# Kernel optimization log

Measured on AMD Instinct MI355X. Metric: run time of the kernel, lower is better.

## Reference

```python
import jax, jax.numpy as jnp
import numpy as np

N = 100000      # nodes
E = 800000      # edges
P = 200000      # number of subgraph permutations
L = 16          # lrp_length
D = 64          # lrp_out_dim (== lrp_in_dim)
PL = P * L
LEN_SEQ = 4     # int(sqrt(L))
NUM_BOND = 4


def setup_inputs() -> dict:
    key = jax.random.key(0)
    ks = jax.random.split(key, 16)
    inp = {}
    inp["nfeat"] = jax.random.normal(ks[0], (N, D), jnp.float32)
    inp["degs"] = jax.random.uniform(ks[1], (N,), jnp.float32) * 8.0 + 1.0
    inp["n2p_val"] = jnp.ones((PL,), jnp.float32)
    inp["e2p_val"] = jnp.ones((PL,), jnp.float32)
    inp["pool_val"] = jax.random.uniform(ks[2], (P,), jnp.float32)
    inp["weights"] = jax.random.normal(ks[3], (D, D, L), jnp.float32)
    inp["bias"] = jnp.zeros((1, D), jnp.float32)
    inp["w_deg0"] = jax.random.normal(ks[4], (2 * D, LEN_SEQ), jnp.float32) * 0.3
    inp["b_deg0"] = jnp.zeros((2 * D,), jnp.float32)
    inp["w_deg1"] = jax.random.normal(ks[5], (D, 2 * D), jnp.float32) * 0.1
    inp["b_deg1"] = jnp.zeros((D,), jnp.float32)
    inp["w_lin"] = jax.random.normal(ks[6], (D, D), jnp.float32) * 0.1
    inp["b_lin"] = jnp.zeros((D,), jnp.float32)
    inp["bond_emb"] = jax.random.normal(ks[7], (NUM_BOND, D), jnp.float32)
    inp["edge_feat_idx"] = jax.random.randint(ks[8], (E,), 0, NUM_BOND, jnp.int32)
    inp["n2p_row"] = jnp.arange(PL, dtype=jnp.int32)
    inp["n2p_col"] = jax.random.randint(ks[9], (PL,), 0, N, jnp.int32)
    inp["e2p_row"] = jnp.arange(PL, dtype=jnp.int32)
    inp["e2p_col"] = jax.random.randint(ks[10], (PL,), 0, E, jnp.int32)
    inp["pool_row"] = jax.random.randint(ks[11], (P,), 0, N, jnp.int32)
    inp["pool_col"] = jnp.arange(P, dtype=jnp.int32)
    return inp


def _spmm(row, col, val, x, m):
    # COO spmm: out[r] = sum_{nnz with row==r} val * x[col]
    return jax.ops.segment_sum(val[:, None] * x[col], row, num_segments=m)


def reference(nfeat, degs, n2p_val, e2p_val, pool_val, weights, bias,
              w_deg0, b_deg0, w_deg1, b_deg1, w_lin, b_lin, bond_emb,
              edge_feat_idx, n2p_row, n2p_col, e2p_row, e2p_col,
              pool_row, pool_col):
    n = nfeat.shape[0]
    pl = n2p_row.shape[0]
    d = weights.shape[0]
    l = weights.shape[2]
    p = pl // l
    len_seq = int(round(l ** 0.5))

    efeat = bond_emb[edge_feat_idx]                                  # [E, D]
    perm = _spmm(n2p_row, n2p_col, n2p_val, nfeat, pl) \
         + _spmm(e2p_row, e2p_col, e2p_val, efeat, pl)               # [P*L, D]
    deg_perm = _spmm(n2p_row, n2p_col, n2p_val, degs[:, None], pl)   # [P*L, 1]

    x = perm.reshape(p, l, d)                                        # [P, L, D]
    deg_sel = deg_perm.reshape(p, l)[:, ::len_seq + 1]               # [P, len_seq]

    h = jnp.einsum('pab,bca->pc', x, weights) + bias                 # [P, D]
    h = jax.nn.relu(h) @ w_lin.T + b_lin                             # linear(relu(.))

    g = jax.nn.relu(deg_sel @ w_deg0.T + b_deg0) @ w_deg1.T + b_deg1  # [P, D]
    h = h * g

    out = _spmm(pool_row, pool_col, pool_val, h, n)                  # [N, D]
    return out
```

## Files before the change

kernel.cpp:

```cpp
#include <hip/hip_runtime.h>
#include <hip/hip_bf16.h>

typedef __attribute__((ext_vector_type(8))) __bf16 bf16x8;
typedef __attribute__((ext_vector_type(4))) float floatx4;
typedef __attribute__((ext_vector_type(4))) int intx4;

constexpr int N_NODES = 100000;
constexpr int P_PERM  = 200000;

constexpr size_t W2F_OFF  = 0;
constexpr size_t WLF_OFF  = 131072;
constexpr size_t WD1F_OFF = 139264;
constexpr size_t BE_OFF   = 155648;
constexpr size_t NFBF_OFF = 3355648;
constexpr size_t H2_OFF   = 16155648;
constexpr size_t RP_OFF   = 67355648;
constexpr size_t CUR_OFF  = 67755664;
constexpr size_t CIDX_OFF = 68155664;
constexpr size_t CSUM_OFF = 68955664;
constexpr size_t WS_NEED_BF16 = 16155648;
constexpr size_t WS_NEED_CSR  = 68956000;

constexpr int SCAN_CHUNK = 2048;
constexpr int NCHUNK = 49;

__global__ void prep_all_kernel(float4* __restrict__ out,
                                const float* __restrict__ weights,
                                const float* __restrict__ w_lin,
                                const float* __restrict__ w_deg1,
                                const float* __restrict__ nfeat,
                                const int* __restrict__ e2p_col,
                                const int* __restrict__ edge_feat_idx,
                                __bf16* __restrict__ ws_bf,
                                int do_zero_out) {
  int b = blockIdx.x;
  int t = threadIdx.x;
  if (b < 6250) {
    if (do_zero_out) out[b * 256 + t] = make_float4(0.f, 0.f, 0.f, 0.f);
  } else if (b < 6554) {
    int i = (b - 6250) * 256 + t;
    if (i < 65536) {
      int j = i & 7, l = (i >> 3) & 63, ct = (i >> 9) & 3, ks = (i >> 11) & 1, a = i >> 12;
      int k = ks * 32 + (l >> 4) * 8 + j;
      int c = ct * 16 + (l & 15);
      ws_bf[W2F_OFF / 2 + i] = (__bf16)weights[k * 1024 + c * 16 + a];
    } else if (i < 65536 + 4096) {
      int i2 = i - 65536;
      int j = i2 & 7, l = (i2 >> 3) & 63, ct = (i2 >> 9) & 3, ks = (i2 >> 11) & 1;
      int k = ks * 32 + (l >> 4) * 8 + j;
      int c = ct * 16 + (l & 15);
      ws_bf[WLF_OFF / 2 + i2] = (__bf16)w_lin[c * 64 + k];
    } else if (i < 65536 + 4096 + 8192) {
      int i3 = i - 65536 - 4096;
      int j = i3 & 7, l = (i3 >> 3) & 63, ct = (i3 >> 9) & 3, ks = (i3 >> 11) & 3;
      int k = ks * 32 + (l >> 4) * 8 + j;
      int c = ct * 16 + (l & 15);
      ws_bf[WD1F_OFF / 2 + i3] = (__bf16)w_deg1[c * 128 + k];
    }
  } else if (b < 9679) {
    int i = (b - 6554) * 256 + t;
    if (i < N_NODES * 8) {
      float4 a = *(const float4*)(nfeat + (size_t)i * 8);
      float4 c = *(const float4*)(nfeat + (size_t)i * 8 + 4);
      bf16x8 o;
      o[0] = (__bf16)a.x; o[1] = (__bf16)a.y; o[2] = (__bf16)a.z; o[3] = (__bf16)a.w;
      o[4] = (__bf16)c.x; o[5] = (__bf16)c.y; o[6] = (__bf16)c.z; o[7] = (__bf16)c.w;
      *(bf16x8*)(ws_bf + NFBF_OFF / 2 + (size_t)i * 8) = o;
    }
  } else if (b < 12804) {
    int i = (b - 9679) * 256 + t;
    if (i < P_PERM * 4) {
      int4 ec = ((const int4*)e2p_col)[i];
      unsigned v = (unsigned)(edge_feat_idx[ec.x] & 0xff)
                 | ((unsigned)(edge_feat_idx[ec.y] & 0xff) << 8)
                 | ((unsigned)(edge_feat_idx[ec.z] & 0xff) << 16)
                 | ((unsigned)(edge_feat_idx[ec.w] & 0xff) << 24);
      ((unsigned*)((char*)ws_bf + BE_OFF))[i] = v;
    }
  } else {
    int i = (b - 12804) * 256 + t;
    if (i < N_NODES) ((int*)((char*)ws_bf + CUR_OFF))[i] = 0;
  }
}

__global__ void hist_kernel(const int* __restrict__ pool_row, int* __restrict__ hist) {
  int i = blockIdx.x * 256 + threadIdx.x;
  if (i < P_PERM) atomicAdd(&hist[pool_row[i]], 1);
}

__global__ void scan1_kernel(const int* __restrict__ hist, int* __restrict__ csum) {
  __shared__ int red[256];
  int b = blockIdx.x, t = threadIdx.x;
  int s = 0;
  #pragma unroll
  for (int j = 0; j < 8; ++j) {
    int i = b * SCAN_CHUNK + t * 8 + j;
    s += (i < N_NODES) ? hist[i] : 0;
  }
  red[t] = s;
  __syncthreads();
  for (int off = 128; off > 0; off >>= 1) {
    if (t < off) red[t] += red[t + off];
    __syncthreads();
  }
  if (t == 0) csum[b] = red[0];
}

__global__ void scan2_kernel(int* __restrict__ csum, int* __restrict__ row_ptr) {
  if (threadIdx.x == 0) {
    int acc = 0;
    for (int i = 0; i < NCHUNK; ++i) {
      int v = csum[i];
      csum[i] = acc;
      acc += v;
    }
    row_ptr[N_NODES] = acc;
  }
}

__global__ void scan3_kernel(const int* __restrict__ csum,
                             int* __restrict__ hist_cursor,
                             int* __restrict__ row_ptr) {
  __shared__ int sc[257];
  int b = blockIdx.x, t = threadIdx.x;
  int v[8];
  int s = 0;
  #pragma unroll
  for (int j = 0; j < 8; ++j) {
    int i = b * SCAN_CHUNK + t * 8 + j;
    v[j] = (i < N_NODES) ? hist_cursor[i] : 0;
    s += v[j];
  }
  sc[t + 1] = s;
  if (t == 0) sc[0] = 0;
  __syncthreads();
  for (int off = 1; off < 256; off <<= 1) {
    int x = (t >= off) ? sc[t + 1 - off] : 0;
    __syncthreads();
    sc[t + 1] += x;
    __syncthreads();
  }
  int excl = csum[b] + sc[t];
  #pragma unroll
  for (int j = 0; j < 8; ++j) {
    int i = b * SCAN_CHUNK + t * 8 + j;
    if (i < N_NODES) {
      row_ptr[i] = excl;
      hist_cursor[i] = excl;
    }
    excl += v[j];
  }
}

__global__ void scatter_kernel(const int* __restrict__ pool_row,
                               int* __restrict__ cursor,
                               int* __restrict__ cidx) {
  int i = blockIdx.x * 256 + threadIdx.x;
  if (i < P_PERM) {
    int pos = atomicAdd(&cursor[pool_row[i]], 1);
    cidx[pos] = i;
  }
}

__global__ __launch_bounds__(256, 8) void pool_kernel(
    const int* __restrict__ row_ptr, const int* __restrict__ cidx,
    const float* __restrict__ pool_val, const float* __restrict__ h2,
    float* __restrict__ out) {
  int g = blockIdx.x * 256 + threadIdx.x;
  int n = g >> 2, qd = g & 3;
  if (n >= N_NODES) return;
  int s = row_ptr[n], e = row_ptr[n + 1];
  floatx4 a0 = {0,0,0,0}, a1 = {0,0,0,0}, a2 = {0,0,0,0}, a3 = {0,0,0,0};
  for (int i = s; i < e; ++i) {
    int p = cidx[i];
    float pv = pool_val[p];
    const float* hr = h2 + (size_t)p * 64 + qd * 16;
    floatx4 h0 = *(const floatx4*)(hr + 0);
    floatx4 h1 = *(const floatx4*)(hr + 4);
    floatx4 h2v = *(const floatx4*)(hr + 8);
    floatx4 h3 = *(const floatx4*)(hr + 12);
    a0 += pv * h0; a1 += pv * h1; a2 += pv * h2v; a3 += pv * h3;
  }
  float* orow = out + (size_t)n * 64 + qd * 16;
  *(floatx4*)(orow + 0) = a0;
  *(floatx4*)(orow + 4) = a1;
  *(floatx4*)(orow + 8) = a2;
  *(floatx4*)(orow + 12) = a3;
}

template <bool BF16FEAT, bool CSR>
__global__ __launch_bounds__(256, 4) void lrp_mfma_kernel(
    const float* __restrict__ nfeat,
    const float* __restrict__ degs,
    const float* __restrict__ n2p_val,
    const float* __restrict__ e2p_val,
    const float* __restrict__ pool_val,
    const float* __restrict__ bias,
    const float* __restrict__ w_deg0,
    const float* __restrict__ b_deg0,
    const float* __restrict__ b_deg1,
    const float* __restrict__ b_lin,
    const float* __restrict__ bond_emb,
    const int* __restrict__ n2p_col,
    const int* __restrict__ pool_row,
    const __bf16* __restrict__ ws_bf,
    float* __restrict__ h2out,
    float* __restrict__ out) {
  __shared__ __align__(16) char fraglds[2][8192];
  __shared__ __align__(16) __bf16 sbond[4][72];
  __shared__ __align__(16) float swdeg0[128][4];
  __shared__ float sbd0[128];
  __shared__ float sbias[64];
  __shared__ float sblin[64];
  __shared__ float sbd1[64];
  __shared__ __align__(16) __bf16 hs[4][2][16][72];

  const int t = threadIdx.x;
  const int w = t >> 6;
  const int l = t & 63;
  const int m = l & 15;
  const int q = l >> 4;
  const int pbase = blockIdx.x * 128 + w * 32;
  int pb[2] = {pbase, pbase + 16};
  bool valid[2];
  int pbc[2];
  #pragma unroll
  for (int pt = 0; pt < 2; ++pt) {
    valid[pt] = pb[pt] < P_PERM;
    pbc[pt] = valid[pt] ? pb[pt] : (P_PERM - 16);
  }

  if (t < 256) sbond[t >> 6][t & 63] = (__bf16)bond_emb[t];
  if (t < 128) {
    *(float4*)&swdeg0[t][0] = *(const float4*)(w_deg0 + t * 4);
    sbd0[t] = b_deg0[t];
  } else if (t < 192) {
    int c = t - 128;
    sbias[c] = bias[c]; sblin[c] = b_lin[c]; sbd1[c] = b_deg1[c];
  }

  const __bf16* __restrict__ nfbf = ws_bf + NFBF_OFF / 2;
  const bf16x8* __restrict__ WLv  = (const bf16x8*)(ws_bf + WLF_OFF / 2);
  const bf16x8* __restrict__ WD1v = (const bf16x8*)(ws_bf + WD1F_OFF / 2);
  const unsigned* __restrict__ bep = (const unsigned*)((const char*)ws_bf + BE_OFF);
  const char* __restrict__ W2bytes = (const char*)ws_bf + W2F_OFF;

  intx4 nvx[2], evx[2], ncx[2];
  int bex[2];
  #pragma unroll
  for (int pt = 0; pt < 2; ++pt) {
    size_t rb = (size_t)pbc[pt] * 16;
    nvx[pt] = *(const intx4*)(n2p_val + rb + 4 * l);
    evx[pt] = *(const intx4*)(e2p_val + rb + 4 * l);
    ncx[pt] = *(const intx4*)(n2p_col + rb + 4 * l);
    bex[pt] = (int)bep[(size_t)pbc[pt] * 4 + l];
  }
  const int selbase = m * 16;

  auto stage = [&](int a, int buf) {
    #pragma unroll
    for (int j = 0; j < 2; ++j) {
      const char* g = W2bytes + (size_t)a * 8192 + (w * 2 + j) * 1024 + l * 16;
      char* lds = &fraglds[buf][(w * 2 + j) * 1024];
      __builtin_amdgcn_global_load_lds(
          (const __attribute__((address_space(1))) unsigned*)g,
          (__attribute__((address_space(3))) unsigned*)lds, 16, 0, 0);
    }
  };
  auto gath = [&](int nc, bf16x8* g) {
    #pragma unroll
    for (int ks = 0; ks < 2; ++ks) {
      int k0 = ks * 32 + q * 8;
      if (BF16FEAT) {
        g[ks] = *(const bf16x8*)(nfbf + (size_t)nc * 64 + k0);
      } else {
        float4 n0 = *(const float4*)(nfeat + (size_t)nc * 64 + k0);
        float4 n1 = *(const float4*)(nfeat + (size_t)nc * 64 + k0 + 4);
        bf16x8 o;
        o[0] = (__bf16)n0.x; o[1] = (__bf16)n0.y; o[2] = (__bf16)n0.z; o[3] = (__bf16)n0.w;
        o[4] = (__bf16)n1.x; o[5] = (__bf16)n1.y; o[6] = (__bf16)n1.z; o[7] = (__bf16)n1.w;
        g[ks] = o;
      }
    }
  };

  floatx4 acc[2][4] = {};
  float dsreg[2][4];
  float nv0[2], ev0[2];
  int nc0[2], be0[2];
  bf16x8 g_cur[2][2], g_nxt[2][2];

  #pragma unroll
  for (int pt = 0; pt < 2; ++pt) {
    nv0[pt] = __int_as_float(__builtin_amdgcn_ds_bpermute(selbase, nvx[pt][0]));
    ev0[pt] = __int_as_float(__builtin_amdgcn_ds_bpermute(selbase, evx[pt][0]));
    nc0[pt] = __builtin_amdgcn_ds_bpermute(selbase, ncx[pt][0]);
    be0[pt] = (__builtin_amdgcn_ds_bpermute(selbase, bex[pt])) & 0xff;
    gath(nc0[pt], g_cur[pt]);
  }
  stage(0, 0);
  __syncthreads();

  #pragma unroll
  for (int a = 0; a < 16; ++a) {
    const int buf = a & 1;
    float nv1[2], ev1[2];
    int nc1[2], be1[2];
    if (a < 15) {
      const int an = a + 1;
      const int sel1 = selbase + (an >> 2) * 4;
      const int sl = an & 3;
      #pragma unroll
      for (int pt = 0; pt < 2; ++pt) {
        nv1[pt] = __int_as_float(__builtin_amdgcn_ds_bpermute(sel1, nvx[pt][sl]));
        ev1[pt] = __int_as_float(__builtin_amdgcn_ds_bpermute(sel1, evx[pt][sl]));
        nc1[pt] = __builtin_amdgcn_ds_bpermute(sel1, ncx[pt][sl]);
        be1[pt] = (__builtin_amdgcn_ds_bpermute(sel1, bex[pt]) >> (sl * 8)) & 0xff;
      }
      stage(a + 1, buf ^ 1);
      #pragma unroll
      for (int pt = 0; pt < 2; ++pt) gath(nc1[pt], g_nxt[pt]);
    }

    bf16x8 afv[2][2];
    #pragma unroll
    for (int pt = 0; pt < 2; ++pt) {
      #pragma unroll
      for (int ks = 0; ks < 2; ++ks) {
        bf16x8 eb = *(const bf16x8*)&sbond[be0[pt]][ks * 32 + q * 8];
        bf16x8 af;
        #pragma unroll
        for (int j = 0; j < 8; ++j)
          af[j] = (__bf16)fmaf(nv0[pt], (float)g_cur[pt][ks][j],
                               ev0[pt] * (float)eb[j]);
        afv[pt][ks] = af;
      }
    }
    #pragma unroll
    for (int ks = 0; ks < 2; ++ks)
      #pragma unroll
      for (int ct = 0; ct < 4; ++ct) {
        bf16x8 frag = *(const bf16x8*)&fraglds[buf][((ks * 4 + ct) * 64 + l) * 16];
        acc[0][ct] = __builtin_amdgcn_mfma_f32_16x16x32_bf16(afv[0][ks], frag, acc[0][ct], 0, 0, 0);
        acc[1][ct] = __builtin_amdgcn_mfma_f32_16x16x32_bf16(afv[1][ks], frag, acc[1][ct], 0, 0, 0);
      }

    if (a == 0 || a == 5 || a == 10 || a == 15) {
      const int jj = a / 5;
      #pragma unroll
      for (int pt = 0; pt < 2; ++pt)
        dsreg[pt][jj] = nv0[pt] * degs[nc0[pt]];
    }

    if (a < 15) {
      __syncthreads();
      #pragma unroll
      for (int pt = 0; pt < 2; ++pt) {
        nv0[pt] = nv1[pt]; ev0[pt] = ev1[pt]; nc0[pt] = nc1[pt]; be0[pt] = be1[pt];
        g_cur[pt][0] = g_nxt[pt][0]; g_cur[pt][1] = g_nxt[pt][1];
      }
    }
  }

  floatx4 acc2[2][4] = {};
  {
    #pragma unroll
    for (int pt = 0; pt < 2; ++pt)
      #pragma unroll
      for (int ct = 0; ct < 4; ++ct) {
        float bv = sbias[ct * 16 + m];
        #pragma unroll
        for (int rr = 0; rr < 4; ++rr)
          hs[w][pt][q * 4 + rr][ct * 16 + m] =
              (__bf16)fmaxf(acc[pt][ct][rr] + bv, 0.0f);
      }
    #pragma unroll
    for (int pt = 0; pt < 2; ++pt)
      #pragma unroll
      for (int ks = 0; ks < 2; ++ks) {
        bf16x8 af2 = *(const bf16x8*)&hs[w][pt][m][ks * 32 + q * 8];
        #pragma unroll
        for (int ct = 0; ct < 4; ++ct) {
          bf16x8 frag = WLv[(ks * 4 + ct) * 64 + l];
          acc2[pt][ct] = __builtin_amdgcn_mfma_f32_16x16x32_bf16(af2, frag, acc2[pt][ct], 0, 0, 0);
        }
      }
  }

  floatx4 gacc[2][4] = {};
  #pragma unroll
  for (int ks = 0; ks < 4; ++ks) {
    const int k0 = ks * 32 + q * 8;
    bf16x8 af[2];
    #pragma unroll
    for (int j = 0; j < 8; ++j) {
      int k = k0 + j;
      float4 wr = *(const float4*)&swdeg0[k][0];
      float bk = sbd0[k];
      #pragma unroll
      for (int pt = 0; pt < 2; ++pt) {
        float v = bk;
        v = fmaf(dsreg[pt][0], wr.x, v);
        v = fmaf(dsreg[pt][1], wr.y, v);
        v = fmaf(dsreg[pt][2], wr.z, v);
        v = fmaf(dsreg[pt][3], wr.w, v);
        af[pt][j] = (__bf16)fmaxf(v, 0.0f);
      }
    }
    #pragma unroll
    for (int ct = 0; ct < 4; ++ct) {
      bf16x8 frag = WD1v[(ks * 4 + ct) * 64 + l];
      gacc[0][ct] = __builtin_amdgcn_mfma_f32_16x16x32_bf16(af[0], frag, gacc[0][ct], 0, 0, 0);
      gacc[1][ct] = __builtin_amdgcn_mfma_f32_16x16x32_bf16(af[1], frag, gacc[1][ct], 0, 0, 0);
    }
  }

  if (CSR) {
    #pragma unroll
    for (int pt = 0; pt < 2; ++pt) {
      if (!valid[pt]) continue;
      #pragma unroll
      for (int rr = 0; rr < 4; ++rr) {
        float* hrow = h2out + (size_t)(pb[pt] + q * 4 + rr) * 64 + m;
        #pragma unroll
        for (int ct = 0; ct < 4; ++ct) {
          float h2 = (acc2[pt][ct][rr] + sblin[ct * 16 + m]) *
                     (gacc[pt][ct][rr] + sbd1[ct * 16 + m]);
          hrow[ct * 16] = h2;
        }
      }
    }
  } else {
    #pragma unroll
    for (int pt = 0; pt < 2; ++pt) {
      if (!valid[pt]) continue;
      intx4   pr4 = *(const intx4*)(pool_row + pb[pt] + q * 4);
      floatx4 pv4 = *(const floatx4*)(pool_val + pb[pt] + q * 4);
      #pragma unroll
      for (int rr = 0; rr < 4; ++rr) {
        float* orow = out + (size_t)pr4[rr] * 64;
        float pv = pv4[rr];
        #pragma unroll
        for (int ct = 0; ct < 4; ++ct) {
          float h2 = (acc2[pt][ct][rr] + sblin[ct * 16 + m]) *
                     (gacc[pt][ct][rr] + sbd1[ct * 16 + m]);
          atomicAdd(orow + ct * 16 + m, pv * h2);
        }
      }
    }
  }
}

extern "C" void kernel_launch(void* const* d_in, const int* in_sizes, int n_in,
                              void* d_out, int out_size, void* d_ws, size_t ws_size,
                              hipStream_t stream) {
  const float* nfeat    = (const float*)d_in[0];
  const float* degs     = (const float*)d_in[1];
  const float* n2p_val  = (const float*)d_in[2];
  const float* e2p_val  = (const float*)d_in[3];
  const float* pool_val = (const float*)d_in[4];
  const float* weights  = (const float*)d_in[5];
  const float* bias     = (const float*)d_in[6];
  const float* w_deg0   = (const float*)d_in[7];
  const float* b_deg0   = (const float*)d_in[8];
  const float* w_deg1   = (const float*)d_in[9];
  const float* b_deg1   = (const float*)d_in[10];
  const float* w_lin    = (const float*)d_in[11];
  const float* b_lin    = (const float*)d_in[12];
  const float* bond_emb = (const float*)d_in[13];
  const int* edge_feat_idx = (const int*)d_in[14];
  const int* n2p_col    = (const int*)d_in[16];
  const int* e2p_col    = (const int*)d_in[18];
  const int* pool_row   = (const int*)d_in[19];

  float* out = (float*)d_out;
  __bf16* ws_bf = (__bf16*)d_ws;
  char* wsb = (char*)d_ws;

  bool bf16feat = ws_size >= WS_NEED_BF16;
  bool csr = ws_size >= WS_NEED_CSR;

  prep_all_kernel<<<13195, 256, 0, stream>>>((float4*)out, weights, w_lin,
                                             w_deg1, nfeat, e2p_col,
                                             edge_feat_idx, ws_bf, csr ? 0 : 1);

  float* h2buf   = (float*)(wsb + H2_OFF);
  int* row_ptr   = (int*)(wsb + RP_OFF);
  int* cursor    = (int*)(wsb + CUR_OFF);
  int* cidx      = (int*)(wsb + CIDX_OFF);
  int* csum      = (int*)(wsb + CSUM_OFF);

  if (csr) {
    hist_kernel<<<(P_PERM + 255) / 256, 256, 0, stream>>>(pool_row, cursor);
    scan1_kernel<<<NCHUNK, 256, 0, stream>>>(cursor, csum);
    scan2_kernel<<<1, 64, 0, stream>>>(csum, row_ptr);
    scan3_kernel<<<NCHUNK, 256, 0, stream>>>(csum, cursor, row_ptr);
    scatter_kernel<<<(P_PERM + 255) / 256, 256, 0, stream>>>(pool_row, cursor, cidx);
  }

  int grid = (P_PERM + 127) / 128;
  if (csr) {
    if (bf16feat)
      lrp_mfma_kernel<true, true><<<grid, 256, 0, stream>>>(
          nfeat, degs, n2p_val, e2p_val, pool_val, bias, w_deg0, b_deg0,
          b_deg1, b_lin, bond_emb, n2p_col, pool_row, ws_bf, h2buf, out);
    else
      lrp_mfma_kernel<false, true><<<grid, 256, 0, stream>>>(
          nfeat, degs, n2p_val, e2p_val, pool_val, bias, w_deg0, b_deg0,
          b_deg1, b_lin, bond_emb, n2p_col, pool_row, ws_bf, h2buf, out);
    pool_kernel<<<(N_NODES * 4 + 255) / 256, 256, 0, stream>>>(
        row_ptr, cidx, pool_val, h2buf, out);
  } else {
    if (bf16feat)
      lrp_mfma_kernel<true, false><<<grid, 256, 0, stream>>>(
          nfeat, degs, n2p_val, e2p_val, pool_val, bias, w_deg0, b_deg0,
          b_deg1, b_lin, bond_emb, n2p_col, pool_row, ws_bf, h2buf, out);
    else
      lrp_mfma_kernel<false, false><<<grid, 256, 0, stream>>>(
          nfeat, degs, n2p_val, e2p_val, pool_val, bias, w_deg0, b_deg0,
          b_deg1, b_lin, bond_emb, n2p_col, pool_row, ws_bf, h2buf, out);
  }
}
```

Before: 332.2 us.

## Store intermediate h2 in bf16, stage deg1 weights in LDS, fold scan2 into scan3

The intermediate per-permutation result h2 is now written as bf16 through an LDS transpose, using coalesced 16-byte row stores, and the pool kernel reads bf16. This halves the intermediate write and read traffic. The w_deg1 fragments are loaded into LDS once per block with global_load_lds instead of being read from global memory per use. The single-thread scan2 launch is removed: each scan3 block sums the preceding chunk totals itself, and row_ptr[N] is set to P. These changes cut memory traffic and one launch, in exchange for more LDS use per block and bf16 rounding of h2 before pooling.

Result: faster. 322.2 us (-3.0%).

```diff
diff --git a/kernel.cpp b/kernel.cpp
--- a/kernel.cpp
+++ b/kernel.cpp
@@ -14,12 +14,12 @@
 constexpr size_t BE_OFF   = 155648;
 constexpr size_t NFBF_OFF = 3355648;
 constexpr size_t H2_OFF   = 16155648;
-constexpr size_t RP_OFF   = 67355648;
-constexpr size_t CUR_OFF  = 67755664;
-constexpr size_t CIDX_OFF = 68155664;
-constexpr size_t CSUM_OFF = 68955664;
+constexpr size_t RP_OFF   = 41755648;
+constexpr size_t CUR_OFF  = 42155664;
+constexpr size_t CIDX_OFF = 42555664;
+constexpr size_t CSUM_OFF = 43355664;
 constexpr size_t WS_NEED_BF16 = 16155648;
-constexpr size_t WS_NEED_CSR  = 68956000;
+constexpr size_t WS_NEED_CSR  = 43356000;
 
 constexpr int SCAN_CHUNK = 2048;
 constexpr int NCHUNK = 49;
@@ -106,23 +106,18 @@
   if (t == 0) csum[b] = red[0];
 }
 
-__global__ void scan2_kernel(int* __restrict__ csum, int* __restrict__ row_ptr) {
-  if (threadIdx.x == 0) {
-    int acc = 0;
-    for (int i = 0; i < NCHUNK; ++i) {
-      int v = csum[i];
-      csum[i] = acc;
-      acc += v;
-    }
-    row_ptr[N_NODES] = acc;
-  }
-}
-
 __global__ void scan3_kernel(const int* __restrict__ csum,
                              int* __restrict__ hist_cursor,
                              int* __restrict__ row_ptr) {
   __shared__ int sc[257];
+  __shared__ int base;
   int b = blockIdx.x, t = threadIdx.x;
+  if (t == 0) {
+    int acc = 0;
+    for (int i = 0; i < b; ++i) acc += csum[i];
+    base = acc;
+    if (b == 0) row_ptr[N_NODES] = P_PERM;
+  }
   int v[8];
   int s = 0;
   #pragma unroll
@@ -140,7 +135,7 @@
     sc[t + 1] += x;
     __syncthreads();
   }
-  int excl = csum[b] + sc[t];
+  int excl = base + sc[t];
   #pragma unroll
   for (int j = 0; j < 8; ++j) {
     int i = b * SCAN_CHUNK + t * 8 + j;
@@ -164,28 +159,29 @@
 
 __global__ __launch_bounds__(256, 8) void pool_kernel(
     const int* __restrict__ row_ptr, const int* __restrict__ cidx,
-    const float* __restrict__ pool_val, const float* __restrict__ h2,
+    const float* __restrict__ pool_val, const __bf16* __restrict__ h2,
     float* __restrict__ out) {
   int g = blockIdx.x * 256 + threadIdx.x;
   int n = g >> 2, qd = g & 3;
   if (n >= N_NODES) return;
   int s = row_ptr[n], e = row_ptr[n + 1];
-  floatx4 a0 = {0,0,0,0}, a1 = {0,0,0,0}, a2 = {0,0,0,0}, a3 = {0,0,0,0};
+  float a[16] = {};
   for (int i = s; i < e; ++i) {
     int p = cidx[i];
     float pv = pool_val[p];
-    const float* hr = h2 + (size_t)p * 64 + qd * 16;
-    floatx4 h0 = *(const floatx4*)(hr + 0);
-    floatx4 h1 = *(const floatx4*)(hr + 4);
-    floatx4 h2v = *(const floatx4*)(hr + 8);
-    floatx4 h3 = *(const floatx4*)(hr + 12);
-    a0 += pv * h0; a1 += pv * h1; a2 += pv * h2v; a3 += pv * h3;
+    const __bf16* hr = h2 + (size_t)p * 64 + qd * 16;
+    bf16x8 v0 = *(const bf16x8*)hr;
+    bf16x8 v1 = *(const bf16x8*)(hr + 8);
+    #pragma unroll
+    for (int j = 0; j < 8; ++j) {
+      a[j]     += pv * (float)v0[j];
+      a[8 + j] += pv * (float)v1[j];
+    }
   }
   float* orow = out + (size_t)n * 64 + qd * 16;
-  *(floatx4*)(orow + 0) = a0;
-  *(floatx4*)(orow + 4) = a1;
-  *(floatx4*)(orow + 8) = a2;
-  *(floatx4*)(orow + 12) = a3;
+  #pragma unroll
+  for (int j = 0; j < 4; ++j)
+    *(floatx4*)(orow + j * 4) = *(const floatx4*)&a[j * 4];
 }
 
 template <bool BF16FEAT, bool CSR>
@@ -204,16 +200,17 @@
     const int* __restrict__ n2p_col,
     const int* __restrict__ pool_row,
     const __bf16* __restrict__ ws_bf,
-    float* __restrict__ h2out,
+    __bf16* __restrict__ h2out,
     float* __restrict__ out) {
   __shared__ __align__(16) char fraglds[2][8192];
+  __shared__ __align__(16) char swd1[16384];
+  __shared__ __align__(16) __bf16 hs[4][16][72];
   __shared__ __align__(16) __bf16 sbond[4][72];
   __shared__ __align__(16) float swdeg0[128][4];
   __shared__ float sbd0[128];
   __shared__ float sbias[64];
   __shared__ float sblin[64];
   __shared__ float sbd1[64];
-  __shared__ __align__(16) __bf16 hs[4][2][16][72];
 
   const int t = threadIdx.x;
   const int w = t >> 6;
@@ -241,9 +238,18 @@
 
   const __bf16* __restrict__ nfbf = ws_bf + NFBF_OFF / 2;
   const bf16x8* __restrict__ WLv  = (const bf16x8*)(ws_bf + WLF_OFF / 2);
-  const bf16x8* __restrict__ WD1v = (const bf16x8*)(ws_bf + WD1F_OFF / 2);
   const unsigned* __restrict__ bep = (const unsigned*)((const char*)ws_bf + BE_OFF);
   const char* __restrict__ W2bytes = (const char*)ws_bf + W2F_OFF;
+  const char* __restrict__ WD1bytes = (const char*)ws_bf + WD1F_OFF;
+
+  #pragma unroll
+  for (int j = 0; j < 4; ++j) {
+    const char* g = WD1bytes + (w * 4 + j) * 1024 + l * 16;
+    char* lds = &swd1[(w * 4 + j) * 1024];
+    __builtin_amdgcn_global_load_lds(
+        (const __attribute__((address_space(1))) unsigned*)g,
+        (__attribute__((address_space(3))) unsigned*)lds, 16, 0, 0);
+  }
 
   intx4 nvx[2], evx[2], ncx[2];
   int bex[2];
@@ -363,28 +369,25 @@
   }
 
   floatx4 acc2[2][4] = {};
-  {
-    #pragma unroll
-    for (int pt = 0; pt < 2; ++pt)
+  #pragma unroll
+  for (int pt = 0; pt < 2; ++pt) {
+    #pragma unroll
+    for (int ct = 0; ct < 4; ++ct) {
+      float bv = sbias[ct * 16 + m];
+      #pragma unroll
+      for (int rr = 0; rr < 4; ++rr)
+        hs[w][q * 4 + rr][ct * 16 + m] =
+            (__bf16)fmaxf(acc[pt][ct][rr] + bv, 0.0f);
+    }
+    #pragma unroll
+    for (int ks = 0; ks < 2; ++ks) {
+      bf16x8 af2 = *(const bf16x8*)&hs[w][m][ks * 32 + q * 8];
       #pragma unroll
       for (int ct = 0; ct < 4; ++ct) {
-        float bv = sbias[ct * 16 + m];
-        #pragma unroll
-        for (int rr = 0; rr < 4; ++rr)
-          hs[w][pt][q * 4 + rr][ct * 16 + m] =
-              (__bf16)fmaxf(acc[pt][ct][rr] + bv, 0.0f);
-      }
-    #pragma unroll
-    for (int pt = 0; pt < 2; ++pt)
-      #pragma unroll
-      for (int ks = 0; ks < 2; ++ks) {
-        bf16x8 af2 = *(const bf16x8*)&hs[w][pt][m][ks * 32 + q * 8];
-        #pragma unroll
-        for (int ct = 0; ct < 4; ++ct) {
-          bf16x8 frag = WLv[(ks * 4 + ct) * 64 + l];
-          acc2[pt][ct] = __builtin_amdgcn_mfma_f32_16x16x32_bf16(af2, frag, acc2[pt][ct], 0, 0, 0);
-        }
-      }
+        bf16x8 frag = WLv[(ks * 4 + ct) * 64 + l];
+        acc2[pt][ct] = __builtin_amdgcn_mfma_f32_16x16x32_bf16(af2, frag, acc2[pt][ct], 0, 0, 0);
+      }
+    }
   }
 
   floatx4 gacc[2][4] = {};
@@ -409,7 +412,7 @@
     }
     #pragma unroll
     for (int ct = 0; ct < 4; ++ct) {
-      bf16x8 frag = WD1v[(ks * 4 + ct) * 64 + l];
+      bf16x8 frag = *(const bf16x8*)&swd1[((ks * 4 + ct) * 64 + l) * 16];
       gacc[0][ct] = __builtin_amdgcn_mfma_f32_16x16x32_bf16(af[0], frag, gacc[0][ct], 0, 0, 0);
       gacc[1][ct] = __builtin_amdgcn_mfma_f32_16x16x32_bf16(af[1], frag, gacc[1][ct], 0, 0, 0);
     }
@@ -420,14 +423,20 @@
     for (int pt = 0; pt < 2; ++pt) {
       if (!valid[pt]) continue;
       #pragma unroll
-      for (int rr = 0; rr < 4; ++rr) {
-        float* hrow = h2out + (size_t)(pb[pt] + q * 4 + rr) * 64 + m;
+      for (int ct = 0; ct < 4; ++ct) {
+        float bl = sblin[ct * 16 + m];
+        float bd = sbd1[ct * 16 + m];
         #pragma unroll
-        for (int ct = 0; ct < 4; ++ct) {
-          float h2 = (acc2[pt][ct][rr] + sblin[ct * 16 + m]) *
-                     (gacc[pt][ct][rr] + sbd1[ct * 16 + m]);
-          hrow[ct * 16] = h2;
+        for (int rr = 0; rr < 4; ++rr) {
+          float h2v = (acc2[pt][ct][rr] + bl) * (gacc[pt][ct][rr] + bd);
+          hs[w][q * 4 + rr][ct * 16 + m] = (__bf16)h2v;
         }
+      }
+      #pragma unroll
+      for (int pass = 0; pass < 2; ++pass) {
+        int row = pass * 8 + (l >> 3);
+        bf16x8 v = *(const bf16x8*)&hs[w][row][(l & 7) * 8];
+        *(bf16x8*)(h2out + (size_t)(pb[pt] + row) * 64 + (l & 7) * 8) = v;
       }
     }
   } else {
@@ -484,16 +493,15 @@
                                              w_deg1, nfeat, e2p_col,
                                              edge_feat_idx, ws_bf, csr ? 0 : 1);
 
-  float* h2buf   = (float*)(wsb + H2_OFF);
-  int* row_ptr   = (int*)(wsb + RP_OFF);
-  int* cursor    = (int*)(wsb + CUR_OFF);
-  int* cidx      = (int*)(wsb + CIDX_OFF);
-  int* csum      = (int*)(wsb + CSUM_OFF);
+  __bf16* h2buf = (__bf16*)(wsb + H2_OFF);
+  int* row_ptr  = (int*)(wsb + RP_OFF);
+  int* cursor   = (int*)(wsb + CUR_OFF);
+  int* cidx     = (int*)(wsb + CIDX_OFF);
+  int* csum     = (int*)(wsb + CSUM_OFF);
 
   if (csr) {
     hist_kernel<<<(P_PERM + 255) / 256, 256, 0, stream>>>(pool_row, cursor);
     scan1_kernel<<<NCHUNK, 256, 0, stream>>>(cursor, csum);
-    scan2_kernel<<<1, 64, 0, stream>>>(csum, row_ptr);
     scan3_kernel<<<NCHUNK, 256, 0, stream>>>(csum, cursor, row_ptr);
     scatter_kernel<<<(P_PERM + 255) / 256, 256, 0, stream>>>(pool_row, cursor, cidx);
   }
```
